# Kernel tuning notes

Hardware: AMD Instinct MI355X
Metric: run time of the kernel (lower is better)

Reference implementation:

```python
import jax, jax.numpy as jnp
import numpy as np

EPS = 1e-12  # matches torch F.normalize eps
TEMPERATURE = 1.0


def _l2_normalize(x):
    n = jnp.sqrt(jnp.sum(x * x, axis=-1, keepdims=True))
    return x / jnp.maximum(n, EPS)


def setup_inputs() -> dict:
    key = jax.random.key(0)
    k1, k2 = jax.random.split(key)
    B, L, D, V = 2, 2048, 1024, 32000
    embeddings = jax.random.normal(k1, (B, L, D), dtype=jnp.float32)
    vocab_embeddings = jax.random.normal(k2, (V, D), dtype=jnp.float32)
    return {"embeddings": embeddings, "vocab_embeddings": vocab_embeddings, "k": 8}


def reference(embeddings, vocab_embeddings, k):
    """Soft KNN routing: cosine similarity -> top-k -> temperature softmax
    scattered into a full (B, L, V) probability distribution, plus hard
    argmax token ids (forward())."""
    B, L, D = embeddings.shape
    V = vocab_embeddings.shape[0]
    q = _l2_normalize(embeddings.reshape(-1, D))          # (N, D)
    vocab = _l2_normalize(vocab_embeddings)               # (V, D)
    sims = q @ vocab.T                                    # (N, V) cosine similarities
    topk_sim, topk_idx = jax.lax.top_k(sims, k)           # (N, k)
    probs_k = jax.nn.softmax(topk_sim / TEMPERATURE, axis=-1)
    N = q.shape[0]
    probs = jnp.zeros((N, V), dtype=probs_k.dtype)
    probs = probs.at[jnp.arange(N)[:, None], topk_idx].set(probs_k)
    probs = probs.reshape(B, L, V)                        # forward_soft output
    token_ids = topk_idx[:, 0].reshape(B, L)              # forward() hard routing (k=1)
    return probs, token_ids
```

## Files before the change

kernel.cpp:

```cpp
#include <hip/hip_runtime.h>
#include <math.h>

typedef unsigned short u16;
typedef unsigned int u32;
typedef float f32x16 __attribute__((ext_vector_type(16)));
typedef short bf16x8 __attribute__((ext_vector_type(8)));
typedef u16 u16x4 __attribute__((ext_vector_type(4)));

static constexpr int N = 4096;
static constexpr int D = 1024;
static constexpr int V = 32000;
static constexpr int K = 8;
static constexpr int BM = 128;
static constexpr int BV = 256;
static constexpr int BK = 64;
static constexpr int NTILES = V / BV;
static constexpr int NG = 16;
static constexpr int NCAND = NG * K;
static constexpr int T16 = 16;
static constexpr int CPL = NCAND / 64;
static constexpr int GRID = (N / BM) * NG;
static constexpr u32 PSENT = 0x00800000u;

static constexpr size_t OUT_PROB_BYTES = (size_t)N * V * 4;
static constexpr size_t CAND_OFS = 83886080;
static constexpr size_t ZOFS = CAND_OFS + (size_t)N * NCAND * 4;
static constexpr size_t NZ4 = (OUT_PROB_BYTES - ZOFS) / 16;

static_assert(N % BM == 0 && V % BV == 0, "tiling");
static_assert(ZOFS % 16 == 0, "align");
static_assert(NZ4 == (size_t)209 * GRID * 256, "zero quota exact");

__device__ __forceinline__ u16 f2bf(float f) {
  u32 u = __float_as_uint(f);
  return (u16)((u + 0x7fffu + ((u >> 16) & 1u)) >> 16);
}
__device__ __forceinline__ u32 flipbits(float v) {
  u32 u = __float_as_uint(v);
  return u ^ (((u32)((int)u >> 31)) | 0x80000000u);
}
__device__ __forceinline__ float unpackval(u32 p) {
  u32 s = p | 2047u;
  u32 u = (s & 0x80000000u) ? (s ^ 0x80000000u) : ~s;
  return __uint_as_float(u);
}
__device__ __forceinline__ void insert8(u32 pv[K], u32 x) {
  if (x <= pv[K - 1]) return;
  bool g[K];
#pragma unroll
  for (int j = 0; j < K; ++j) g[j] = x > pv[j];
#pragma unroll
  for (int j = K - 1; j >= 1; --j)
    pv[j] = g[j - 1] ? pv[j - 1] : (g[j] ? x : pv[j]);
  if (g[0]) pv[0] = x;
}

__global__ void zero_kernel(float4* __restrict__ p, int n4) {
  int i = blockIdx.x * blockDim.x + threadIdx.x;
  int stride = gridDim.x * blockDim.x;
  float4 z = make_float4(0.f, 0.f, 0.f, 0.f);
  for (; i < n4; i += stride) p[i] = z;
}

__global__ void normcvt_kernel(const float* __restrict__ x, float* __restrict__ inv,
                               u16* __restrict__ o) {
  int row = blockIdx.x;
  const float4* xr = reinterpret_cast<const float4*>(x + (size_t)row * D);
  float4 v = xr[threadIdx.x];
  float ss = v.x * v.x + v.y * v.y + v.z * v.z + v.w * v.w;
#pragma unroll
  for (int off = 32; off > 0; off >>= 1) ss += __shfl_down(ss, off, 64);
  __shared__ float wsum[4];
  if ((threadIdx.x & 63) == 0) wsum[threadIdx.x >> 6] = ss;
  __syncthreads();
  __shared__ float s_inv;
  if (threadIdx.x == 0) {
    float t = wsum[0] + wsum[1] + wsum[2] + wsum[3];
    float iv = 1.0f / fmaxf(sqrtf(t), 1e-12f);
    inv[row] = iv;
    s_inv = iv;
  }
  __syncthreads();
  float s = s_inv;
  u16x4 r;
  r[0] = f2bf(v.x * s); r[1] = f2bf(v.y * s); r[2] = f2bf(v.z * s); r[3] = f2bf(v.w * s);
  *reinterpret_cast<u16x4*>(o + (size_t)row * D + threadIdx.x * 4) = r;
}

__global__ __launch_bounds__(256, 2)
void simtopk_kernel(const u16* __restrict__ qn, const u16* __restrict__ vn,
                    u32* __restrict__ cand, float4* __restrict__ zout) {
  __shared__ __align__(16) u16 sh[(BV + BM) * BK];

  u16* v_sh = sh;
  u16* q_sh = sh + BV * BK;

  const int tid = threadIdx.x;
  const int bid = blockIdx.x;
  const int u_ = bid >> 3;
  const int rb = u_ & 31;
  const int grp = (bid & 7) * 2 + (u_ >> 5);
  const int t0 = (grp * NTILES) >> 4;
  const int t1 = ((grp + 1) * NTILES) >> 4;
  const int rbase = rb * BM;
  const int wid = tid >> 6, l = tid & 63;
  const int wv = wid >> 1, wq = wid & 1;
  const int h = l >> 5, lid = l & 31;
  const int sk = (((l & 7) ^ (l >> 3)) << 3);

  const float4 zf4 = make_float4(0.f, 0.f, 0.f, 0.f);

  u32 pv[2][K];
#pragma unroll
  for (int n = 0; n < 2; ++n)
#pragma unroll
    for (int j = 0; j < K; ++j) pv[n][j] = PSENT;
  float tminf[2] = {-3.0e38f, -3.0e38f};

  for (int ti = t0; ti < t1; ++ti) {
    const int cb = (ti - t0) * BV;
    f32x16 acc[4][2];
#pragma unroll
    for (int m = 0; m < 4; ++m)
#pragma unroll
      for (int n = 0; n < 2; ++n)
#pragma unroll
        for (int r = 0; r < 16; ++r) acc[m][n][r] = 0.f;

    for (int kk = 0; kk < D / BK; ++kk) {
      __syncthreads();
      {
        int it = (ti - t0) * 16 + kk;
#pragma unroll
        for (int j = 0; j < 2; ++j) {
          int s = it * 2 + j;
          if (s < 209) zout[(size_t)s * (GRID * 256) + bid * 256 + tid] = zf4;
        }
      }
      const int kbase = kk * BK;
#pragma unroll
      for (int c = 0; c < 8; ++c) {
        int seg = c * 4 + wid;
        int vrow = seg * 8 + (l >> 3);
        const u16* gs = vn + (size_t)(ti * BV + vrow) * D + kbase + sk;
        __builtin_amdgcn_global_load_lds((const __attribute__((address_space(1))) void*)gs,
            (__attribute__((address_space(3))) void*)(v_sh + seg * 512), 16, 0, 0);
      }
#pragma unroll
      for (int c = 0; c < 4; ++c) {
        int seg = c * 4 + wid;
        int qrow = seg * 8 + (l >> 3);
        const u16* gs = qn + (size_t)(rbase + qrow) * D + kbase + sk;
        __builtin_amdgcn_global_load_lds((const __attribute__((address_space(1))) void*)gs,
            (__attribute__((address_space(3))) void*)(q_sh + seg * 512), 16, 0, 0);
      }
      __syncthreads();
      __builtin_amdgcn_s_setprio(1);
#pragma unroll
      for (int t = 0; t < 4; ++t) {
        const int ch = t * 2 + h;
        bf16x8 vf[4], qf[2];
#pragma unroll
        for (int m = 0; m < 4; ++m) {
          int row = wv * 128 + m * 32 + lid;
          vf[m] = *reinterpret_cast<const bf16x8*>(v_sh + row * BK + ((ch ^ (row & 7)) << 3));
        }
#pragma unroll
        for (int n = 0; n < 2; ++n) {
          int row = wq * 64 + n * 32 + lid;
          qf[n] = *reinterpret_cast<const bf16x8*>(q_sh + row * BK + ((ch ^ (row & 7)) << 3));
        }
#pragma unroll
        for (int m = 0; m < 4; ++m)
#pragma unroll
          for (int n = 0; n < 2; ++n)
            acc[m][n] = __builtin_amdgcn_mfma_f32_32x32x16_bf16(vf[m], qf[n], acc[m][n], 0, 0, 0);
      }
      __builtin_amdgcn_s_setprio(0);
    }

#pragma unroll
    for (int n = 0; n < 2; ++n) {
#pragma unroll
      for (int m = 0; m < 4; ++m) {
        f32x16 a = acc[m][n];
        float x01 = fmaxf(a[0], a[1]),   x23 = fmaxf(a[2], a[3]);
        float x45 = fmaxf(a[4], a[5]),   x67 = fmaxf(a[6], a[7]);
        float x89 = fmaxf(a[8], a[9]),   xab = fmaxf(a[10], a[11]);
        float xcd = fmaxf(a[12], a[13]), xef = fmaxf(a[14], a[15]);
        float mx = fmaxf(fmaxf(fmaxf(x01, x23), fmaxf(x45, x67)),
                         fmaxf(fmaxf(x89, xab), fmaxf(xcd, xef)));
        if (mx > tminf[n]) {
          const int cidb = cb + wv * 128 + m * 32 + 4 * h;
#pragma unroll
          for (int r = 0; r < 16; ++r) {
            float v = a[r];
            if (v > tminf[n]) {
              int cid = cidb + (r & 3) + 8 * (r >> 2);
              u32 p = (flipbits(v) & 0xFFFFF800u) | (u32)(2047 - cid);
              insert8(pv[n], p);
            }
          }
          tminf[n] = unpackval(pv[n][K - 1]);
        }
      }
    }
  }

  __syncthreads();
  u32* marr = (u32*)sh;
#pragma unroll
  for (int n = 0; n < 2; ++n)
#pragma unroll
    for (int j = 0; j < K; ++j)
      marr[((wq * 64 + n * 32 + lid) * 4 + (wv * 2 + h)) * K + j] = pv[n][j];
  __syncthreads();
  if (tid < BM) {
    u32 fv[K];
#pragma unroll
    for (int j = 0; j < K; ++j) fv[j] = PSENT;
#pragma unroll
    for (int c4 = 0; c4 < 4; ++c4)
#pragma unroll
      for (int j = 0; j < K; ++j) insert8(fv, marr[(tid * 4 + c4) * K + j]);
#pragma unroll
    for (int j = 0; j < K; ++j)
      cand[(size_t)(rbase + tid) * NCAND + grp * K + j] = fv[j];
  }
}

__global__ __launch_bounds__(256)
void rescore_kernel(const u32* __restrict__ cand,
                    const float* __restrict__ emb, const float* __restrict__ vocab,
                    const float* __restrict__ invq, const float* __restrict__ invv,
                    float* __restrict__ res_p, int* __restrict__ res_i) {
  const int tid = threadIdx.x, wid = tid >> 6, l = tid & 63;
  const int row = blockIdx.x * 4 + wid;

  float4 q[4];
#pragma unroll
  for (int t = 0; t < 4; ++t)
    q[t] = *(reinterpret_cast<const float4*>(emb + (size_t)row * D) + t * 64 + l);
  float iqr = invq[row];

  u32 pl[CPL]; int li[CPL];
#pragma unroll
  for (int t = 0; t < CPL; ++t) {
    int e = l * CPL + t;
    u32 p = cand[(size_t)row * NCAND + e];
    int grp = e >> 3;
    int tile0 = (grp * NTILES) >> 4;
    pl[t] = p;
    li[t] = tile0 * BV + 2047 - (int)(p & 2047u);
  }

  int cidx[T16];
#pragma unroll
  for (int jr = 0; jr < T16; ++jr) {
    u32 bp = pl[0]; int bi = li[0];
#pragma unroll
    for (int t = 1; t < CPL; ++t)
      if (pl[t] > bp || (pl[t] == bp && li[t] < bi)) { bp = pl[t]; bi = li[t]; }
#pragma unroll
    for (int off = 32; off > 0; off >>= 1) {
      u32 op = (u32)__shfl_xor((int)bp, off, 64); int oi = __shfl_xor(bi, off, 64);
      if (op > bp || (op == bp && oi < bi)) { bp = op; bi = oi; }
    }
    cidx[jr] = bi;
#pragma unroll
    for (int t = 0; t < CPL; ++t) if (li[t] == bi) pl[t] = 0u;
  }

  float sv[T16];
#pragma unroll
  for (int jr = 0; jr < T16; ++jr) {
    int ix = cidx[jr];
    const float4* vr = reinterpret_cast<const float4*>(vocab + (size_t)ix * D);
    float s = 0.f;
#pragma unroll
    for (int t = 0; t < 4; ++t) {
      float4 vv = vr[t * 64 + l];
      s += q[t].x * vv.x + q[t].y * vv.y + q[t].z * vv.z + q[t].w * vv.w;
    }
#pragma unroll
    for (int off = 32; off > 0; off >>= 1) s += __shfl_xor(s, off, 64);
    sv[jr] = s * iqr * invv[ix];
  }

  float pvv[K]; int pii[K];
#pragma unroll
  for (int r8 = 0; r8 < K; ++r8) {
    float bv = sv[0]; int bi = cidx[0];
#pragma unroll
    for (int jr = 1; jr < T16; ++jr)
      if (sv[jr] > bv || (sv[jr] == bv && cidx[jr] < bi)) { bv = sv[jr]; bi = cidx[jr]; }
    pvv[r8] = bv; pii[r8] = bi;
#pragma unroll
    for (int jr = 0; jr < T16; ++jr) if (cidx[jr] == bi) sv[jr] = -3.0e38f;
  }

  float m = pvv[0], sum = 0.f, e8[K];
#pragma unroll
  for (int j = 0; j < K; ++j) { e8[j] = expf(pvv[j] - m); sum += e8[j]; }
  float isum = 1.f / sum;
  if (l == 0) {
#pragma unroll
    for (int j = 0; j < K; ++j) {
      res_p[row * K + j] = e8[j] * isum;
      res_i[row * K + j] = pii[j];
    }
  }
}

__global__ void scatter_kernel(const float* __restrict__ res_p, const int* __restrict__ res_i,
                               float* __restrict__ out) {
  int row = blockIdx.x * blockDim.x + threadIdx.x;
#pragma unroll
  for (int j = 0; j < K; ++j) out[(size_t)row * V + res_i[row * K + j]] = res_p[row * K + j];
  out[(size_t)N * V + row] = (float)res_i[row * K];
}

extern "C" void kernel_launch(void* const* d_in, const int* in_sizes, int n_in,
                              void* d_out, int out_size, void* d_ws, size_t ws_size,
                              hipStream_t stream) {
  const float* emb   = (const float*)d_in[0];
  const float* vocab = (const float*)d_in[1];
  float* out = (float*)d_out;

  u16* qn = (u16*)d_out;
  u16* vn = qn + (size_t)N * D;
  u32* cand = (u32*)((char*)d_out + CAND_OFS);
  float4* ztail = (float4*)((char*)d_out + ZOFS);

  float* wsf   = (float*)d_ws;
  float* invq  = wsf;
  float* invv  = wsf + N;
  float* res_p = wsf + N + V;
  int*   res_i = (int*)(wsf + N + V + N * K);

  normcvt_kernel<<<N, 256, 0, stream>>>(emb, invq, qn);
  normcvt_kernel<<<V, 256, 0, stream>>>(vocab, invv, vn);
  simtopk_kernel<<<GRID, 256, 0, stream>>>(qn, vn, cand, ztail);
  rescore_kernel<<<N / 4, 256, 0, stream>>>(cand, emb, vocab, invq, invv, res_p, res_i);
  zero_kernel<<<2048, 256, 0, stream>>>((float4*)d_out, (int)(ZOFS / 16));
  scatter_kernel<<<N / 256, 256, 0, stream>>>(res_p, res_i, out);
}
```

Baseline: 519.4 us.

## Switch candidate similarity GEMM from bf16 to fp8 MFMA

Normalized query and vocab vectors are now quantized to scaled fp8 (e4m3) instead of bf16, and the similarity GEMM uses the 32x32x16 fp8 MFMA with byte-sized LDS tiles and a new swizzle. This halves the bytes loaded and staged per tile and uses the higher-throughput fp8 matrix path. The coarser similarities only pick candidates, which are then rescored exactly in fp32, but precision loss could push a true top-k entry out of the candidate set.

```diff
diff --git a/kernel.cpp b/kernel.cpp
--- a/kernel.cpp
+++ b/kernel.cpp
@@ -3,9 +3,9 @@
 
 typedef unsigned short u16;
 typedef unsigned int u32;
+typedef unsigned char u8;
+typedef long i64;
 typedef float f32x16 __attribute__((ext_vector_type(16)));
-typedef short bf16x8 __attribute__((ext_vector_type(8)));
-typedef u16 u16x4 __attribute__((ext_vector_type(4)));
 
 static constexpr int N = 4096;
 static constexpr int D = 1024;
@@ -31,9 +31,18 @@
 static_assert(ZOFS % 16 == 0, "align");
 static_assert(NZ4 == (size_t)209 * GRID * 256, "zero quota exact");
 
-__device__ __forceinline__ u16 f2bf(float f) {
+__device__ __forceinline__ u8 f2fp8(float f) {
   u32 u = __float_as_uint(f);
-  return (u16)((u + 0x7fffu + ((u >> 16) & 1u)) >> 16);
+  u32 sign = (u >> 24) & 0x80u;
+  u32 au = u & 0x7FFFFFFFu;
+  if (au < 0x3C000000u) {
+    int m = (int)(__uint_as_float(au) * 512.0f + 0.5f);
+    return (u8)(sign | (u32)m);
+  }
+  au += 0x7FFFFu + ((au >> 20) & 1u);
+  if (au >= 0x43E00000u) return (u8)(sign | 0x7Eu);
+  u32 e = (au >> 23) - 120u;
+  return (u8)(sign | (e << 3) | ((au >> 20) & 7u));
 }
 __device__ __forceinline__ u32 flipbits(float v) {
   u32 u = __float_as_uint(v);
@@ -63,7 +72,7 @@
 }
 
 __global__ void normcvt_kernel(const float* __restrict__ x, float* __restrict__ inv,
-                               u16* __restrict__ o) {
+                               u32* __restrict__ o) {
   int row = blockIdx.x;
   const float4* xr = reinterpret_cast<const float4*>(x + (size_t)row * D);
   float4 v = xr[threadIdx.x];
@@ -81,19 +90,18 @@
     s_inv = iv;
   }
   __syncthreads();
-  float s = s_inv;
-  u16x4 r;
-  r[0] = f2bf(v.x * s); r[1] = f2bf(v.y * s); r[2] = f2bf(v.z * s); r[3] = f2bf(v.w * s);
-  *reinterpret_cast<u16x4*>(o + (size_t)row * D + threadIdx.x * 4) = r;
+  float s = s_inv * 16.0f;
+  u32 b0 = f2fp8(v.x * s), b1 = f2fp8(v.y * s), b2 = f2fp8(v.z * s), b3 = f2fp8(v.w * s);
+  o[row * (D / 4) + threadIdx.x] = b0 | (b1 << 8) | (b2 << 16) | (b3 << 24);
 }
 
 __global__ __launch_bounds__(256, 2)
-void simtopk_kernel(const u16* __restrict__ qn, const u16* __restrict__ vn,
+void simtopk_kernel(const u8* __restrict__ qn, const u8* __restrict__ vn,
                     u32* __restrict__ cand, float4* __restrict__ zout) {
-  __shared__ __align__(16) u16 sh[(BV + BM) * BK];
-
-  u16* v_sh = sh;
-  u16* q_sh = sh + BV * BK;
+  __shared__ __align__(16) u8 sh[(BV + BM) * BK];
+
+  u8* v_sh = sh;
+  u8* q_sh = sh + BV * BK;
 
   const int tid = threadIdx.x;
   const int bid = blockIdx.x;
@@ -106,7 +114,8 @@
   const int wid = tid >> 6, l = tid & 63;
   const int wv = wid >> 1, wq = wid & 1;
   const int h = l >> 5, lid = l & 31;
-  const int sk = (((l & 7) ^ (l >> 3)) << 3);
+  const int srow = l >> 2;
+  const int sk = ((l & 3) ^ (srow & 3)) << 4;
 
   const float4 zf4 = make_float4(0.f, 0.f, 0.f, 0.f);
 
@@ -137,44 +146,44 @@
           if (s < 209) zout[(size_t)s * (GRID * 256) + bid * 256 + tid] = zf4;
         }
       }
-      const int kbase = kk * BK;
-#pragma unroll
-      for (int c = 0; c < 8; ++c) {
-        int seg = c * 4 + wid;
-        int vrow = seg * 8 + (l >> 3);
-        const u16* gs = vn + (size_t)(ti * BV + vrow) * D + kbase + sk;
-        __builtin_amdgcn_global_load_lds((const __attribute__((address_space(1))) void*)gs,
-            (__attribute__((address_space(3))) void*)(v_sh + seg * 512), 16, 0, 0);
-      }
+      const int kb = kk * BK;
 #pragma unroll
       for (int c = 0; c < 4; ++c) {
         int seg = c * 4 + wid;
-        int qrow = seg * 8 + (l >> 3);
-        const u16* gs = qn + (size_t)(rbase + qrow) * D + kbase + sk;
+        const u8* gs = vn + (size_t)(ti * BV + seg * 16 + srow) * D + kb + sk;
         __builtin_amdgcn_global_load_lds((const __attribute__((address_space(1))) void*)gs,
-            (__attribute__((address_space(3))) void*)(q_sh + seg * 512), 16, 0, 0);
+            (__attribute__((address_space(3))) void*)(v_sh + seg * 1024), 16, 0, 0);
+      }
+#pragma unroll
+      for (int c = 0; c < 2; ++c) {
+        int seg = c * 4 + wid;
+        const u8* gs = qn + (size_t)(rbase + seg * 16 + srow) * D + kb + sk;
+        __builtin_amdgcn_global_load_lds((const __attribute__((address_space(1))) void*)gs,
+            (__attribute__((address_space(3))) void*)(q_sh + seg * 1024), 16, 0, 0);
       }
       __syncthreads();
       __builtin_amdgcn_s_setprio(1);
 #pragma unroll
       for (int t = 0; t < 4; ++t) {
         const int ch = t * 2 + h;
-        bf16x8 vf[4], qf[2];
+        i64 vf[4], qf[2];
 #pragma unroll
         for (int m = 0; m < 4; ++m) {
           int row = wv * 128 + m * 32 + lid;
-          vf[m] = *reinterpret_cast<const bf16x8*>(v_sh + row * BK + ((ch ^ (row & 7)) << 3));
+          int byte = row * BK + ((((ch >> 1) ^ (row & 3)) << 4) | ((ch & 1) << 3));
+          vf[m] = *reinterpret_cast<const i64*>(v_sh + byte);
         }
 #pragma unroll
         for (int n = 0; n < 2; ++n) {
           int row = wq * 64 + n * 32 + lid;
-          qf[n] = *reinterpret_cast<const bf16x8*>(q_sh + row * BK + ((ch ^ (row & 7)) << 3));
+          int byte = row * BK + ((((ch >> 1) ^ (row & 3)) << 4) | ((ch & 1) << 3));
+          qf[n] = *reinterpret_cast<const i64*>(q_sh + byte);
         }
 #pragma unroll
         for (int m = 0; m < 4; ++m)
 #pragma unroll
           for (int n = 0; n < 2; ++n)
-            acc[m][n] = __builtin_amdgcn_mfma_f32_32x32x16_bf16(vf[m], qf[n], acc[m][n], 0, 0, 0);
+            acc[m][n] = __builtin_amdgcn_mfma_f32_32x32x16_fp8_fp8(vf[m], qf[n], acc[m][n], 0, 0, 0);
       }
       __builtin_amdgcn_s_setprio(0);
     }
@@ -327,8 +336,8 @@
   const float* vocab = (const float*)d_in[1];
   float* out = (float*)d_out;
 
-  u16* qn = (u16*)d_out;
-  u16* vn = qn + (size_t)N * D;
+  u8* qn = (u8*)d_out;
+  u8* vn = qn + (size_t)N * D;
   u32* cand = (u32*)((char*)d_out + CAND_OFS);
   float4* ztail = (float4*)((char*)d_out + ZOFS);
 
@@ -338,8 +347,8 @@
   float* res_p = wsf + N + V;
   int*   res_i = (int*)(wsf + N + V + N * K);
 
-  normcvt_kernel<<<N, 256, 0, stream>>>(emb, invq, qn);
-  normcvt_kernel<<<V, 256, 0, stream>>>(vocab, invv, vn);
+  normcvt_kernel<<<N, 256, 0, stream>>>(emb, invq, (u32*)qn);
+  normcvt_kernel<<<V, 256, 0, stream>>>(vocab, invv, (u32*)vn);
   simtopk_kernel<<<GRID, 256, 0, stream>>>(qn, vn, cand, ztail);
   rescore_kernel<<<N / 4, 256, 0, stream>>>(cand, emb, vocab, invq, invv, res_p, res_i);
   zero_kernel<<<2048, 256, 0, stream>>>((float4*)d_out, (int)(ZOFS / 16));
```

New measurement: 490.9 us. 5.5% less time.
